# Kernel tuning notes

Hardware: AMD Instinct MI355X
Metric: run time of the kernel (lower is better)

The kernel has to match this reference:

```python
import jax, jax.numpy as jnp
import numpy as np

N, F_IN, F_OUT, N_HEAD = 4096, 256, 64, 4
EDGE_P = 0.01  # sparsity of the random adjacency


def setup_inputs() -> dict:
    key = jax.random.key(0)
    k_h, k_adj, k_w, k_as, k_ad = jax.random.split(key, 5)
    h = jax.random.normal(k_h, (N, F_IN), dtype=jnp.float32)
    # random boolean adjacency with self-loops so every softmax row is valid
    adj = jax.random.uniform(k_adj, (N, N)) < EDGE_P
    adj = adj | jnp.eye(N, dtype=bool)
    # xavier_uniform-style params
    lim_w = float(np.sqrt(6.0 / (F_IN + F_OUT)))
    lim_a = float(np.sqrt(6.0 / (F_OUT + 1)))
    w = jax.random.uniform(k_w, (N_HEAD, F_IN, F_OUT), minval=-lim_w, maxval=lim_w, dtype=jnp.float32)
    a_src = jax.random.uniform(k_as, (N_HEAD, F_OUT, 1), minval=-lim_a, maxval=lim_a, dtype=jnp.float32)
    a_dst = jax.random.uniform(k_ad, (N_HEAD, F_OUT, 1), minval=-lim_a, maxval=lim_a, dtype=jnp.float32)
    bias = jnp.zeros((F_OUT,), dtype=jnp.float32)
    return {"h": h, "adj": adj, "w": w, "a_src": a_src, "a_dst": a_dst, "bias": bias}


def reference(h, adj, w, a_src, a_dst, bias):
    # h_prime[k] = h @ w[k]  -> [H, n, f_out]
    h_prime = jnp.einsum('nf,hfo->hno', h, w)
    # attention logits: attn[k,i,j] = src[k,i] + dst[k,j]
    src = jnp.einsum('hno,ho->hn', h_prime, a_src[..., 0])  # [H, n]
    dst = jnp.einsum('hno,ho->hn', h_prime, a_dst[..., 0])  # [H, n]
    scores = src[:, :, None] + dst[:, None, :]              # [H, n, n]
    scores = jnp.where(scores >= 0, scores, 0.2 * scores)   # leaky_relu(0.2)
    neg = jnp.asarray(jnp.finfo(scores.dtype).min, scores.dtype)
    scores = jnp.where(adj[None, :, :], scores, neg)
    attn = jax.nn.softmax(scores, axis=-1)                  # [H, n, n]
    out = jnp.einsum('hij,hjo->iho', attn, h_prime)         # [n, H, f_out]
    return out + bias
```

## Files before the change

kernel.cpp:

```cpp
#include <hip/hip_runtime.h>

#define NN 4096
#define FIN 256
#define FOUT 64
#define NH 4
#define CAP 128
#define WROW 258

typedef __attribute__((ext_vector_type(8))) short bf16x8;
typedef __attribute__((ext_vector_type(4))) float f32x4;

__device__ __forceinline__ unsigned short f2bf(float f) {
    unsigned u = __float_as_uint(f);
    u = (u + 0x7fff + ((u >> 16) & 1)) >> 16;
    return (unsigned short)u;
}
__device__ __forceinline__ float bf2f(unsigned short s) {
    return __uint_as_float((unsigned)s << 16);
}
__device__ __forceinline__ int mbcnt64(unsigned long long m) {
    return __builtin_amdgcn_mbcnt_hi((unsigned)(m >> 32),
           __builtin_amdgcn_mbcnt_lo((unsigned)m, 0));
}

__global__ __launch_bounds__(256) void gat_hprime(
    const float* __restrict__ h, const float* __restrict__ w,
    const float* __restrict__ a_src, const float* __restrict__ a_dst,
    unsigned short* __restrict__ hb, float* __restrict__ sd)
{
    const int b = blockIdx.x, t = threadIdx.x;
    const int head = b & 3, n0 = (b >> 2) * 32;
    const int wv = t >> 6, lane = t & 63;
    const int lrow = lane & 15, lk8 = lane >> 4;

    __shared__ __align__(16) unsigned short ws[64 * WROW];
    __shared__ float sdbuf[2][2][16][2];

#pragma unroll
    for (int i = 0; i < 16; ++i) {
        const int k  = (t >> 4) + i * 16;
        const int o4 = (t & 15) * 4;
        const float4 v = *(const float4*)(w + ((size_t)head * FIN + k) * FOUT + o4);
        ws[(o4 + 0) * WROW + k] = f2bf(v.x);
        ws[(o4 + 1) * WROW + k] = f2bf(v.y);
        ws[(o4 + 2) * WROW + k] = f2bf(v.z);
        ws[(o4 + 3) * WROW + k] = f2bf(v.w);
    }

    const float* hrow = h + (size_t)(n0 + (wv >> 1) * 16 + lrow) * FIN + lk8 * 8;
    bf16x8 a[8];
#pragma unroll
    for (int ks = 0; ks < 8; ++ks) {
        const float4 v0 = *(const float4*)(hrow + ks * 32);
        const float4 v1 = *(const float4*)(hrow + ks * 32 + 4);
        union { bf16x8 v; unsigned short s[8]; } u;
        u.s[0] = f2bf(v0.x); u.s[1] = f2bf(v0.y);
        u.s[2] = f2bf(v0.z); u.s[3] = f2bf(v0.w);
        u.s[4] = f2bf(v1.x); u.s[5] = f2bf(v1.y);
        u.s[6] = f2bf(v1.z); u.s[7] = f2bf(v1.w);
        a[ks] = u.v;
    }
    __syncthreads();

    const int obase = (wv & 1) * 32;
    f32x4 acc[2] = {{0.f,0.f,0.f,0.f},{0.f,0.f,0.f,0.f}};
#pragma unroll
    for (int ks = 0; ks < 8; ++ks) {
#pragma unroll
        for (int nt = 0; nt < 2; ++nt) {
            const bf16x8 bf = *(const bf16x8*)
                &ws[(obase + nt * 16 + lrow) * WROW + ks * 32 + lk8 * 8];
            acc[nt] = __builtin_amdgcn_mfma_f32_16x16x32_bf16(a[ks], bf, acc[nt], 0, 0, 0);
        }
    }

    const int mbase = n0 + (wv >> 1) * 16 + lk8 * 4;
#pragma unroll
    for (int nt = 0; nt < 2; ++nt)
#pragma unroll
        for (int r = 0; r < 4; ++r)
            hb[((size_t)head * NN + mbase + r) * FOUT + obase + nt * 16 + lrow] =
                f2bf(acc[nt][r]);

    float as_nt[2], ad_nt[2];
#pragma unroll
    for (int nt = 0; nt < 2; ++nt) {
        as_nt[nt] = a_src[head * FOUT + obase + nt * 16 + lrow];
        ad_nt[nt] = a_dst[head * FOUT + obase + nt * 16 + lrow];
    }
    float psr[4] = {0.f,0.f,0.f,0.f}, pdr[4] = {0.f,0.f,0.f,0.f};
#pragma unroll
    for (int nt = 0; nt < 2; ++nt)
#pragma unroll
        for (int r = 0; r < 4; ++r) {
            psr[r] = fmaf(acc[nt][r], as_nt[nt], psr[r]);
            pdr[r] = fmaf(acc[nt][r], ad_nt[nt], pdr[r]);
        }
#pragma unroll
    for (int r = 0; r < 4; ++r)
#pragma unroll
        for (int off = 1; off <= 8; off <<= 1) {
            psr[r] += __shfl_xor(psr[r], off, 64);
            pdr[r] += __shfl_xor(pdr[r], off, 64);
        }
    if (lrow == 0)
#pragma unroll
        for (int r = 0; r < 4; ++r) {
            sdbuf[wv >> 1][wv & 1][lk8 * 4 + r][0] = psr[r];
            sdbuf[wv >> 1][wv & 1][lk8 * 4 + r][1] = pdr[r];
        }
    __syncthreads();
    if ((wv & 1) == 0 && lrow == 0) {
        const int p = wv >> 1;
#pragma unroll
        for (int r = 0; r < 4; ++r) {
            const int n = lk8 * 4 + r;
            const int node = n0 + p * 16 + n;
            sd[(size_t)node * 8 + head]     = sdbuf[p][0][n][0] + sdbuf[p][1][n][0];
            sd[(size_t)node * 8 + 4 + head] = sdbuf[p][0][n][1] + sdbuf[p][1][n][1];
        }
    }
}

__global__ __launch_bounds__(256) void gat_attn(
    const int* __restrict__ adj, const unsigned short* __restrict__ hb,
    const float* __restrict__ sd, const float* __restrict__ bias,
    float* __restrict__ out)
{
    const int i = blockIdx.x, t = threadIdx.x, wv = t >> 6, lane = t & 63;

    __shared__ int   idx_l[CAP];
    __shared__ float sc[NH][CAP];
    __shared__ int   ccnt[16];
    __shared__ float inv_sum[NH];

    const int4* arow = (const int4*)(adj + (size_t)i * NN);
    int4 a[4];
#pragma unroll
    for (int it = 0; it < 4; ++it) a[it] = arow[wv * 256 + it * 64 + lane];

    int myoff[4];
#pragma unroll
    for (int it = 0; it < 4; ++it) {
        const unsigned long long b0 = __ballot(a[it].x != 0);
        const unsigned long long b1 = __ballot(a[it].y != 0);
        const unsigned long long b2 = __ballot(a[it].z != 0);
        const unsigned long long b3 = __ballot(a[it].w != 0);
        myoff[it] = mbcnt64(b0) + mbcnt64(b1) + mbcnt64(b2) + mbcnt64(b3);
        if (lane == 0)
            ccnt[wv * 4 + it] = __popcll(b0) + __popcll(b1) +
                                __popcll(b2) + __popcll(b3);
    }
    __syncthreads();

    int cb[4];
    int s = 0;
#pragma unroll
    for (int k = 0; k < 16; ++k) {
        if ((k >> 2) == wv) cb[k & 3] = s;
        s += ccnt[k];
    }
    const int count = min(s, CAP);
    const int cpad  = (count + 7) & ~7;

#pragma unroll
    for (int it = 0; it < 4; ++it) {
        int p = cb[it] + myoff[it];
        const int col0 = (wv * 256 + it * 64 + lane) * 4;
        if (a[it].x) { if (p < CAP) idx_l[p] = col0;     ++p; }
        if (a[it].y) { if (p < CAP) idx_l[p] = col0 + 1; ++p; }
        if (a[it].z) { if (p < CAP) idx_l[p] = col0 + 2; ++p; }
        if (a[it].w) { if (p < CAP) idx_l[p] = col0 + 3; ++p; }
    }
    __syncthreads();

    if (t < count) {
        const int j = idx_l[t];
        const float4 sv = *(const float4*)(sd + (size_t)i * 8);
        const float4 dv = *(const float4*)(sd + (size_t)j * 8 + 4);
        const float s0 = sv.x + dv.x, s1 = sv.y + dv.y;
        const float s2 = sv.z + dv.z, s3 = sv.w + dv.w;
        sc[0][t] = (s0 >= 0.f) ? s0 : 0.2f * s0;
        sc[1][t] = (s1 >= 0.f) ? s1 : 0.2f * s1;
        sc[2][t] = (s2 >= 0.f) ? s2 : 0.2f * s2;
        sc[3][t] = (s3 >= 0.f) ? s3 : 0.2f * s3;
    } else if (t < cpad) {
        idx_l[t] = 0;
#pragma unroll
        for (int hh = 0; hh < NH; ++hh) sc[hh][t] = 0.f;
    }
    __syncthreads();

    {
        float m = -3.4e38f;
        for (int p = lane; p < count; p += 64) m = fmaxf(m, sc[wv][p]);
#pragma unroll
        for (int off = 32; off >= 1; off >>= 1) m = fmaxf(m, __shfl_xor(m, off, 64));
        float e = 0.f;
        for (int p = lane; p < count; p += 64) {
            const float v = __expf(sc[wv][p] - m);
            sc[wv][p] = v;
            e += v;
        }
#pragma unroll
        for (int off = 32; off >= 1; off >>= 1) e += __shfl_xor(e, off, 64);
        if (lane == 0) inv_sum[wv] = 1.f / e;
    }
    __syncthreads();

    float accv = 0.f;
    const unsigned short* hp = hb + (size_t)(wv * NN) * FOUT + lane;
    for (int p0 = 0; p0 < cpad; p0 += 8) {
        int jj[8]; unsigned short vv[8]; float ww[8];
#pragma unroll
        for (int k = 0; k < 8; ++k) jj[k] = idx_l[p0 + k];
#pragma unroll
        for (int k = 0; k < 8; ++k) vv[k] = hp[(size_t)jj[k] * FOUT];
#pragma unroll
        for (int k = 0; k < 8; ++k) ww[k] = sc[wv][p0 + k];
#pragma unroll
        for (int k = 0; k < 8; ++k) accv = fmaf(ww[k], bf2f(vv[k]), accv);
    }
    out[(size_t)i * (NH * FOUT) + wv * FOUT + lane] = accv * inv_sum[wv] + bias[lane];
}

extern "C" void kernel_launch(void* const* d_in, const int* in_sizes, int n_in,
                              void* d_out, int out_size, void* d_ws, size_t ws_size,
                              hipStream_t stream) {
    const float* h     = (const float*)d_in[0];
    const int*   adj   = (const int*)d_in[1];
    const float* w     = (const float*)d_in[2];
    const float* a_src = (const float*)d_in[3];
    const float* a_dst = (const float*)d_in[4];
    const float* bias  = (const float*)d_in[5];
    float* out = (float*)d_out;

    unsigned short* hb = (unsigned short*)d_ws;
    float* sd          = (float*)(hb + (size_t)NH * NN * FOUT);

    gat_hprime<<<512, 256, 0, stream>>>(h, w, a_src, a_dst, hb, sd);
    gat_attn<<<NN, 256, 0, stream>>>(adj, hb, sd, bias, out);
}
```

Before: 36.15 us.

## Process one attention row per wavefront and drop block-wide barriers

```diff
diff --git a/kernel.cpp b/kernel.cpp
--- a/kernel.cpp
+++ b/kernel.cpp
@@ -127,101 +127,110 @@
     const float* __restrict__ sd, const float* __restrict__ bias,
     float* __restrict__ out)
 {
-    const int i = blockIdx.x, t = threadIdx.x, wv = t >> 6, lane = t & 63;
-
-    __shared__ int   idx_l[CAP];
-    __shared__ float sc[NH][CAP];
-    __shared__ int   ccnt[16];
-    __shared__ float inv_sum[NH];
+    const int t = threadIdx.x, wv = t >> 6, lane = t & 63;
+    const int i = blockIdx.x * 4 + wv;
+
+    __shared__ int   idx_l[4][CAP];
+    __shared__ float scpk[4][CAP][4];
 
     const int4* arow = (const int4*)(adj + (size_t)i * NN);
-    int4 a[4];
-#pragma unroll
-    for (int it = 0; it < 4; ++it) a[it] = arow[wv * 256 + it * 64 + lane];
-
-    int myoff[4];
-#pragma unroll
-    for (int it = 0; it < 4; ++it) {
-        const unsigned long long b0 = __ballot(a[it].x != 0);
-        const unsigned long long b1 = __ballot(a[it].y != 0);
-        const unsigned long long b2 = __ballot(a[it].z != 0);
-        const unsigned long long b3 = __ballot(a[it].w != 0);
-        myoff[it] = mbcnt64(b0) + mbcnt64(b1) + mbcnt64(b2) + mbcnt64(b3);
-        if (lane == 0)
-            ccnt[wv * 4 + it] = __popcll(b0) + __popcll(b1) +
-                                __popcll(b2) + __popcll(b3);
-    }
-    __syncthreads();
-
-    int cb[4];
-    int s = 0;
-#pragma unroll
-    for (int k = 0; k < 16; ++k) {
-        if ((k >> 2) == wv) cb[k & 3] = s;
-        s += ccnt[k];
-    }
-    const int count = min(s, CAP);
-    const int cpad  = (count + 7) & ~7;
-
-#pragma unroll
-    for (int it = 0; it < 4; ++it) {
-        int p = cb[it] + myoff[it];
-        const int col0 = (wv * 256 + it * 64 + lane) * 4;
-        if (a[it].x) { if (p < CAP) idx_l[p] = col0;     ++p; }
-        if (a[it].y) { if (p < CAP) idx_l[p] = col0 + 1; ++p; }
-        if (a[it].z) { if (p < CAP) idx_l[p] = col0 + 2; ++p; }
-        if (a[it].w) { if (p < CAP) idx_l[p] = col0 + 3; ++p; }
-    }
-    __syncthreads();
-
-    if (t < count) {
-        const int j = idx_l[t];
-        const float4 sv = *(const float4*)(sd + (size_t)i * 8);
-        const float4 dv = *(const float4*)(sd + (size_t)j * 8 + 4);
-        const float s0 = sv.x + dv.x, s1 = sv.y + dv.y;
-        const float s2 = sv.z + dv.z, s3 = sv.w + dv.w;
-        sc[0][t] = (s0 >= 0.f) ? s0 : 0.2f * s0;
-        sc[1][t] = (s1 >= 0.f) ? s1 : 0.2f * s1;
-        sc[2][t] = (s2 >= 0.f) ? s2 : 0.2f * s2;
-        sc[3][t] = (s3 >= 0.f) ? s3 : 0.2f * s3;
-    } else if (t < cpad) {
-        idx_l[t] = 0;
-#pragma unroll
-        for (int hh = 0; hh < NH; ++hh) sc[hh][t] = 0.f;
-    }
-    __syncthreads();
-
+    int run = 0;
+#pragma unroll
+    for (int half = 0; half < 2; ++half) {
+        int4 v[8];
+#pragma unroll
+        for (int it = 0; it < 8; ++it) v[it] = arow[(half * 8 + it) * 64 + lane];
+#pragma unroll
+        for (int it = 0; it < 8; ++it) {
+            const unsigned long long b0 = __ballot(v[it].x != 0);
+            const unsigned long long b1 = __ballot(v[it].y != 0);
+            const unsigned long long b2 = __ballot(v[it].z != 0);
+            const unsigned long long b3 = __ballot(v[it].w != 0);
+            int p = run + mbcnt64(b0) + mbcnt64(b1) + mbcnt64(b2) + mbcnt64(b3);
+            const int col0 = ((half * 8 + it) * 64 + lane) * 4;
+            if (v[it].x) { if (p < CAP) idx_l[wv][p] = col0;     ++p; }
+            if (v[it].y) { if (p < CAP) idx_l[wv][p] = col0 + 1; ++p; }
+            if (v[it].z) { if (p < CAP) idx_l[wv][p] = col0 + 2; ++p; }
+            if (v[it].w) { if (p < CAP) idx_l[wv][p] = col0 + 3; ++p; }
+            run += __popcll(b0) + __popcll(b1) + __popcll(b2) + __popcll(b3);
+        }
+    }
+    const int count = min(run, CAP);
+    asm volatile("" ::: "memory");
+
+    const float4 sv = *(const float4*)(sd + (size_t)i * 8);
+    const bool actA = lane < count, actB = lane + 64 < count;
+    const int jA = actA ? idx_l[wv][lane] : 0;
+    const int jB = actB ? idx_l[wv][lane + 64] : 0;
+    const float4 dvA = *(const float4*)(sd + (size_t)jA * 8 + 4);
+    const float4 dvB = *(const float4*)(sd + (size_t)jB * 8 + 4);
+
+    float sA[4], sB[4];
     {
-        float m = -3.4e38f;
-        for (int p = lane; p < count; p += 64) m = fmaxf(m, sc[wv][p]);
-#pragma unroll
-        for (int off = 32; off >= 1; off >>= 1) m = fmaxf(m, __shfl_xor(m, off, 64));
-        float e = 0.f;
-        for (int p = lane; p < count; p += 64) {
-            const float v = __expf(sc[wv][p] - m);
-            sc[wv][p] = v;
-            e += v;
-        }
-#pragma unroll
-        for (int off = 32; off >= 1; off >>= 1) e += __shfl_xor(e, off, 64);
-        if (lane == 0) inv_sum[wv] = 1.f / e;
-    }
-    __syncthreads();
-
-    float accv = 0.f;
-    const unsigned short* hp = hb + (size_t)(wv * NN) * FOUT + lane;
-    for (int p0 = 0; p0 < cpad; p0 += 8) {
-        int jj[8]; unsigned short vv[8]; float ww[8];
-#pragma unroll
-        for (int k = 0; k < 8; ++k) jj[k] = idx_l[p0 + k];
-#pragma unroll
-        for (int k = 0; k < 8; ++k) vv[k] = hp[(size_t)jj[k] * FOUT];
-#pragma unroll
-        for (int k = 0; k < 8; ++k) ww[k] = sc[wv][p0 + k];
-#pragma unroll
-        for (int k = 0; k < 8; ++k) accv = fmaf(ww[k], bf2f(vv[k]), accv);
-    }
-    out[(size_t)i * (NH * FOUT) + wv * FOUT + lane] = accv * inv_sum[wv] + bias[lane];
+        const float a0 = sv.x + dvA.x, a1 = sv.y + dvA.y,
+                    a2 = sv.z + dvA.z, a3 = sv.w + dvA.w;
+        const float b0 = sv.x + dvB.x, b1 = sv.y + dvB.y,
+                    b2 = sv.z + dvB.z, b3 = sv.w + dvB.w;
+        sA[0] = actA ? ((a0 >= 0.f) ? a0 : 0.2f * a0) : -3.4e38f;
+        sA[1] = actA ? ((a1 >= 0.f) ? a1 : 0.2f * a1) : -3.4e38f;
+        sA[2] = actA ? ((a2 >= 0.f) ? a2 : 0.2f * a2) : -3.4e38f;
+        sA[3] = actA ? ((a3 >= 0.f) ? a3 : 0.2f * a3) : -3.4e38f;
+        sB[0] = actB ? ((b0 >= 0.f) ? b0 : 0.2f * b0) : -3.4e38f;
+        sB[1] = actB ? ((b1 >= 0.f) ? b1 : 0.2f * b1) : -3.4e38f;
+        sB[2] = actB ? ((b2 >= 0.f) ? b2 : 0.2f * b2) : -3.4e38f;
+        sB[3] = actB ? ((b3 >= 0.f) ? b3 : 0.2f * b3) : -3.4e38f;
+    }
+
+    float m[4], eA[4], eB[4], inv[4];
+#pragma unroll
+    for (int hh = 0; hh < 4; ++hh) {
+        float mm = fmaxf(sA[hh], sB[hh]);
+#pragma unroll
+        for (int off = 32; off >= 1; off >>= 1)
+            mm = fmaxf(mm, __shfl_xor(mm, off, 64));
+        m[hh] = mm;
+        eA[hh] = actA ? __expf(sA[hh] - mm) : 0.f;
+        eB[hh] = actB ? __expf(sB[hh] - mm) : 0.f;
+        float e = eA[hh] + eB[hh];
+#pragma unroll
+        for (int off = 32; off >= 1; off >>= 1)
+            e += __shfl_xor(e, off, 64);
+        inv[hh] = 1.f / e;
+    }
+
+    if (actA) *(float4*)&scpk[wv][lane][0]      = make_float4(eA[0], eA[1], eA[2], eA[3]);
+    if (actB) *(float4*)&scpk[wv][lane + 64][0] = make_float4(eB[0], eB[1], eB[2], eB[3]);
+    asm volatile("" ::: "memory");
+
+    float acc[4] = {0.f, 0.f, 0.f, 0.f};
+    const unsigned short* hpb = hb + lane;
+    for (int p0 = 0; p0 < count; p0 += 4) {
+        int jj[4]; float wts[4][4]; unsigned short hv[4][4];
+#pragma unroll
+        for (int k = 0; k < 4; ++k) {
+            const int pp = p0 + k;
+            const bool act = pp < count;
+            jj[k] = act ? idx_l[wv][pp] : 0;
+            const float4 wt = act ? *(const float4*)&scpk[wv][pp][0]
+                                  : make_float4(0.f, 0.f, 0.f, 0.f);
+            wts[k][0] = wt.x; wts[k][1] = wt.y; wts[k][2] = wt.z; wts[k][3] = wt.w;
+        }
+#pragma unroll
+        for (int k = 0; k < 4; ++k)
+#pragma unroll
+            for (int hh = 0; hh < 4; ++hh)
+                hv[k][hh] = hpb[((size_t)(hh * NN) + jj[k]) * FOUT];
+#pragma unroll
+        for (int k = 0; k < 4; ++k)
+#pragma unroll
+            for (int hh = 0; hh < 4; ++hh)
+                acc[hh] = fmaf(wts[k][hh], bf2f(hv[k][hh]), acc[hh]);
+    }
+
+    const float bv = bias[lane];
+#pragma unroll
+    for (int hh = 0; hh < 4; ++hh)
+        out[(size_t)i * (NH * FOUT) + hh * FOUT + lane] = acc[hh] * inv[hh] + bv;
 }
 
 extern "C" void kernel_launch(void* const* d_in, const int* in_sizes, int n_in,
@@ -239,5 +248,5 @@
     float* sd          = (float*)(hb + (size_t)NH * NN * FOUT);
 
     gat_hprime<<<512, 256, 0, stream>>>(h, w, a_src, a_dst, hb, sd);
-    gat_attn<<<NN, 256, 0, stream>>>(adj, hb, sd, bias, out);
-}
+    gat_attn<<<NN / 4, 256, 0, stream>>>(adj, hb, sd, bias, out);
+}
```

Measured after the change: 39.19 us. +8.4%, slower.

## Split neighbor aggregation across waves with vectorized 4-wide bf16 gathers and LDS reduction

Applied to the files above, without the earlier changes.

```diff
diff --git a/kernel.cpp b/kernel.cpp
--- a/kernel.cpp
+++ b/kernel.cpp
@@ -133,6 +133,7 @@
     __shared__ float sc[NH][CAP];
     __shared__ int   ccnt[16];
     __shared__ float inv_sum[NH];
+    __shared__ float accbuf[4][64][4];
 
     const int4* arow = (const int4*)(adj + (size_t)i * NN);
     int4 a[4];
@@ -161,7 +162,6 @@
         s += ccnt[k];
     }
     const int count = min(s, CAP);
-    const int cpad  = (count + 7) & ~7;
 
 #pragma unroll
     for (int it = 0; it < 4; ++it) {
@@ -184,10 +184,6 @@
         sc[1][t] = (s1 >= 0.f) ? s1 : 0.2f * s1;
         sc[2][t] = (s2 >= 0.f) ? s2 : 0.2f * s2;
         sc[3][t] = (s3 >= 0.f) ? s3 : 0.2f * s3;
-    } else if (t < cpad) {
-        idx_l[t] = 0;
-#pragma unroll
-        for (int hh = 0; hh < NH; ++hh) sc[hh][t] = 0.f;
     }
     __syncthreads();
 
@@ -208,20 +204,50 @@
     }
     __syncthreads();
 
-    float accv = 0.f;
-    const unsigned short* hp = hb + (size_t)(wv * NN) * FOUT + lane;
-    for (int p0 = 0; p0 < cpad; p0 += 8) {
-        int jj[8]; unsigned short vv[8]; float ww[8];
-#pragma unroll
-        for (int k = 0; k < 8; ++k) jj[k] = idx_l[p0 + k];
-#pragma unroll
-        for (int k = 0; k < 8; ++k) vv[k] = hp[(size_t)jj[k] * FOUT];
-#pragma unroll
-        for (int k = 0; k < 8; ++k) ww[k] = sc[wv][p0 + k];
-#pragma unroll
-        for (int k = 0; k < 8; ++k) accv = fmaf(ww[k], bf2f(vv[k]), accv);
-    }
-    out[(size_t)i * (NH * FOUT) + wv * FOUT + lane] = accv * inv_sum[wv] + bias[lane];
+    const int hh = lane >> 4, og = lane & 15;
+    const unsigned short* hpb = hb + (size_t)hh * NN * FOUT + og * 4;
+    float4 accv = make_float4(0.f, 0.f, 0.f, 0.f);
+    for (int p0 = wv; p0 < count; p0 += 16) {
+        int jj[4]; float ee[4]; ushort4 hv[4];
+#pragma unroll
+        for (int k = 0; k < 4; ++k) {
+            const int pp = p0 + k * 4;
+            const bool act = pp < count;
+            jj[k] = act ? idx_l[pp] : 0;
+            ee[k] = act ? sc[hh][pp] : 0.f;
+        }
+#pragma unroll
+        for (int k = 0; k < 4; ++k)
+            hv[k] = *(const ushort4*)(hpb + (size_t)jj[k] * FOUT);
+#pragma unroll
+        for (int k = 0; k < 4; ++k) {
+            accv.x = fmaf(ee[k], bf2f(hv[k].x), accv.x);
+            accv.y = fmaf(ee[k], bf2f(hv[k].y), accv.y);
+            accv.z = fmaf(ee[k], bf2f(hv[k].z), accv.z);
+            accv.w = fmaf(ee[k], bf2f(hv[k].w), accv.w);
+        }
+    }
+    *(float4*)&accbuf[wv][lane][0] = accv;
+    __syncthreads();
+
+    if (wv == 0) {
+        float4 r0 = *(const float4*)&accbuf[0][lane][0];
+        const float4 r1 = *(const float4*)&accbuf[1][lane][0];
+        const float4 r2 = *(const float4*)&accbuf[2][lane][0];
+        const float4 r3 = *(const float4*)&accbuf[3][lane][0];
+        r0.x += r1.x + r2.x + r3.x;
+        r0.y += r1.y + r2.y + r3.y;
+        r0.z += r1.z + r2.z + r3.z;
+        r0.w += r1.w + r2.w + r3.w;
+        const float is = inv_sum[hh];
+        const float4 bv = *(const float4*)(bias + og * 4);
+        float4 o;
+        o.x = r0.x * is + bv.x;
+        o.y = r0.y * is + bv.y;
+        o.z = r0.z * is + bv.z;
+        o.w = r0.w * is + bv.w;
+        *(float4*)(out + (size_t)i * (NH * FOUT) + hh * FOUT + og * 4) = o;
+    }
 }
 
 extern "C" void kernel_launch(void* const* d_in, const int* in_sizes, int n_in,
```

After: 34.65 us. 1.04x faster.

## Process four rows per attention block with double-buffered adjacency prefetch

Applied to the files above, without the earlier changes.

```diff
diff --git a/kernel.cpp b/kernel.cpp
--- a/kernel.cpp
+++ b/kernel.cpp
@@ -21,6 +21,10 @@
 __device__ __forceinline__ int mbcnt64(unsigned long long m) {
     return __builtin_amdgcn_mbcnt_hi((unsigned)(m >> 32),
            __builtin_amdgcn_mbcnt_lo((unsigned)m, 0));
+}
+__device__ __forceinline__ void wg_barrier() {
+    asm volatile("s_waitcnt lgkmcnt(0)" ::: "memory");
+    __builtin_amdgcn_s_barrier();
 }
 
 __global__ __launch_bounds__(256) void gat_hprime(
@@ -122,106 +126,148 @@
     }
 }
 
+#define LOADROW(BUF, RR) do {                                              \
+    const int4* arow_ = (const int4*)(adj + (size_t)(RR) * NN);            \
+    _Pragma("unroll")                                                      \
+    for (int it_ = 0; it_ < 4; ++it_)                                      \
+        BUF[it_] = arow_[wv * 256 + it_ * 64 + lane];                      \
+} while (0)
+
+#define TAIL(BUF, RR) do {                                                 \
+    int myoff_[4];                                                         \
+    _Pragma("unroll")                                                      \
+    for (int it_ = 0; it_ < 4; ++it_) {                                    \
+        const unsigned long long b0_ = __ballot(BUF[it_].x != 0);          \
+        const unsigned long long b1_ = __ballot(BUF[it_].y != 0);          \
+        const unsigned long long b2_ = __ballot(BUF[it_].z != 0);          \
+        const unsigned long long b3_ = __ballot(BUF[it_].w != 0);          \
+        myoff_[it_] = mbcnt64(b0_) + mbcnt64(b1_) + mbcnt64(b2_) + mbcnt64(b3_); \
+        if (lane == 0)                                                     \
+            ccnt[wv * 4 + it_] = __popcll(b0_) + __popcll(b1_) +           \
+                                 __popcll(b2_) + __popcll(b3_);            \
+    }                                                                      \
+    wg_barrier();                                                          \
+    int cb_[4];                                                            \
+    int s_ = 0;                                                            \
+    _Pragma("unroll")                                                      \
+    for (int k_ = 0; k_ < 16; ++k_) {                                      \
+        if ((k_ >> 2) == wv) cb_[k_ & 3] = s_;                             \
+        s_ += ccnt[k_];                                                    \
+    }                                                                      \
+    const int count_ = min(s_, CAP);                                       \
+    _Pragma("unroll")                                                      \
+    for (int it_ = 0; it_ < 4; ++it_) {                                    \
+        int p_ = cb_[it_] + myoff_[it_];                                   \
+        const int col0_ = (wv * 256 + it_ * 64 + lane) * 4;                \
+        if (BUF[it_].x) { if (p_ < CAP) idx_l[p_] = col0_;     ++p_; }     \
+        if (BUF[it_].y) { if (p_ < CAP) idx_l[p_] = col0_ + 1; ++p_; }     \
+        if (BUF[it_].z) { if (p_ < CAP) idx_l[p_] = col0_ + 2; ++p_; }     \
+        if (BUF[it_].w) { if (p_ < CAP) idx_l[p_] = col0_ + 3; ++p_; }     \
+    }                                                                      \
+    wg_barrier();                                                          \
+    if (t < count_) {                                                      \
+        const int j_ = idx_l[t];                                           \
+        const float4 sv_ = *(const float4*)(sd + (size_t)(RR) * 8);        \
+        const float4 dv_ = *(const float4*)(sd + (size_t)j_ * 8 + 4);      \
+        const float s0_ = sv_.x + dv_.x, s1_ = sv_.y + dv_.y;              \
+        const float s2_ = sv_.z + dv_.z, s3_ = sv_.w + dv_.w;              \
+        sc[0][t] = (s0_ >= 0.f) ? s0_ : 0.2f * s0_;                        \
+        sc[1][t] = (s1_ >= 0.f) ? s1_ : 0.2f * s1_;                        \
+        sc[2][t] = (s2_ >= 0.f) ? s2_ : 0.2f * s2_;                        \
+        sc[3][t] = (s3_ >= 0.f) ? s3_ : 0.2f * s3_;                        \
+    }                                                                      \
+    wg_barrier();                                                          \
+    {                                                                      \
+        float m_ = -3.4e38f;                                               \
+        for (int p_ = lane; p_ < count_; p_ += 64)                         \
+            m_ = fmaxf(m_, sc[wv][p_]);                                    \
+        _Pragma("unroll")                                                  \
+        for (int off_ = 32; off_ >= 1; off_ >>= 1)                         \
+            m_ = fmaxf(m_, __shfl_xor(m_, off_, 64));                      \
+        float e_ = 0.f;                                                    \
+        for (int p_ = lane; p_ < count_; p_ += 64) {                       \
+            const float v_ = __expf(sc[wv][p_] - m_);                      \
+            sc[wv][p_] = v_;                                               \
+            e_ += v_;                                                      \
+        }                                                                  \
+        _Pragma("unroll")                                                  \
+        for (int off_ = 32; off_ >= 1; off_ >>= 1)                         \
+            e_ += __shfl_xor(e_, off_, 64);                                \
+        if (lane == 0) inv_sum[wv] = 1.f / e_;                             \
+    }                                                                      \
+    wg_barrier();                                                          \
+    {                                                                      \
+        const int hh_ = lane >> 4, og_ = lane & 15;                        \
+        const unsigned short* hpb_ = hb + (size_t)hh_ * NN * FOUT + og_ * 4; \
+        float4 accv_ = make_float4(0.f, 0.f, 0.f, 0.f);                    \
+        for (int p0_ = wv; p0_ < count_; p0_ += 16) {                      \
+            int jj_[4]; float ee_[4]; ushort4 hv_[4];                      \
+            _Pragma("unroll")                                              \
+            for (int k_ = 0; k_ < 4; ++k_) {                               \
+                const int pp_ = p0_ + k_ * 4;                              \
+                const bool act_ = pp_ < count_;                            \
+                jj_[k_] = act_ ? idx_l[pp_] : 0;                           \
+                ee_[k_] = act_ ? sc[hh_][pp_] : 0.f;                       \
+            }                                                              \
+            _Pragma("unroll")                                              \
+            for (int k_ = 0; k_ < 4; ++k_)                                 \
+                hv_[k_] = *(const ushort4*)(hpb_ + (size_t)jj_[k_] * FOUT); \
+            _Pragma("unroll")                                              \
+            for (int k_ = 0; k_ < 4; ++k_) {                               \
+                accv_.x = fmaf(ee_[k_], bf2f(hv_[k_].x), accv_.x);         \
+                accv_.y = fmaf(ee_[k_], bf2f(hv_[k_].y), accv_.y);         \
+                accv_.z = fmaf(ee_[k_], bf2f(hv_[k_].z), accv_.z);         \
+                accv_.w = fmaf(ee_[k_], bf2f(hv_[k_].w), accv_.w);         \
+            }                                                              \
+        }                                                                  \
+        *(float4*)&accbuf[wv][lane][0] = accv_;                            \
+    }                                                                      \
+    wg_barrier();                                                          \
+    if (wv == 0) {                                                         \
+        const int hh_ = lane >> 4, og_ = lane & 15;                        \
+        float4 r0_ = *(const float4*)&accbuf[0][lane][0];                  \
+        const float4 r1_ = *(const float4*)&accbuf[1][lane][0];            \
+        const float4 r2_ = *(const float4*)&accbuf[2][lane][0];            \
+        const float4 r3_ = *(const float4*)&accbuf[3][lane][0];            \
+        r0_.x += r1_.x + r2_.x + r3_.x;                                    \
+        r0_.y += r1_.y + r2_.y + r3_.y;                                    \
+        r0_.z += r1_.z + r2_.z + r3_.z;                                    \
+        r0_.w += r1_.w + r2_.w + r3_.w;                                    \
+        const float is_ = inv_sum[hh_];                                    \
+        const float4 bv_ = *(const float4*)(bias + og_ * 4);               \
+        float4 o_;                                                         \
+        o_.x = r0_.x * is_ + bv_.x;                                        \
+        o_.y = r0_.y * is_ + bv_.y;                                        \
+        o_.z = r0_.z * is_ + bv_.z;                                        \
+        o_.w = r0_.w * is_ + bv_.w;                                        \
+        *(float4*)(out + (size_t)(RR) * (NH * FOUT) + hh_ * FOUT + og_ * 4) = o_; \
+    }                                                                      \
+    wg_barrier();                                                          \
+} while (0)
+
 __global__ __launch_bounds__(256) void gat_attn(
     const int* __restrict__ adj, const unsigned short* __restrict__ hb,
     const float* __restrict__ sd, const float* __restrict__ bias,
     float* __restrict__ out)
 {
-    const int i = blockIdx.x, t = threadIdx.x, wv = t >> 6, lane = t & 63;
+    const int t = threadIdx.x, wv = t >> 6, lane = t & 63;
+    const int r0 = blockIdx.x * 4;
 
     __shared__ int   idx_l[CAP];
     __shared__ float sc[NH][CAP];
     __shared__ int   ccnt[16];
     __shared__ float inv_sum[NH];
-
-    const int4* arow = (const int4*)(adj + (size_t)i * NN);
-    int4 a[4];
-#pragma unroll
-    for (int it = 0; it < 4; ++it) a[it] = arow[wv * 256 + it * 64 + lane];
-
-    int myoff[4];
-#pragma unroll
-    for (int it = 0; it < 4; ++it) {
-        const unsigned long long b0 = __ballot(a[it].x != 0);
-        const unsigned long long b1 = __ballot(a[it].y != 0);
-        const unsigned long long b2 = __ballot(a[it].z != 0);
-        const unsigned long long b3 = __ballot(a[it].w != 0);
-        myoff[it] = mbcnt64(b0) + mbcnt64(b1) + mbcnt64(b2) + mbcnt64(b3);
-        if (lane == 0)
-            ccnt[wv * 4 + it] = __popcll(b0) + __popcll(b1) +
-                                __popcll(b2) + __popcll(b3);
-    }
-    __syncthreads();
-
-    int cb[4];
-    int s = 0;
-#pragma unroll
-    for (int k = 0; k < 16; ++k) {
-        if ((k >> 2) == wv) cb[k & 3] = s;
-        s += ccnt[k];
-    }
-    const int count = min(s, CAP);
-    const int cpad  = (count + 7) & ~7;
-
-#pragma unroll
-    for (int it = 0; it < 4; ++it) {
-        int p = cb[it] + myoff[it];
-        const int col0 = (wv * 256 + it * 64 + lane) * 4;
-        if (a[it].x) { if (p < CAP) idx_l[p] = col0;     ++p; }
-        if (a[it].y) { if (p < CAP) idx_l[p] = col0 + 1; ++p; }
-        if (a[it].z) { if (p < CAP) idx_l[p] = col0 + 2; ++p; }
-        if (a[it].w) { if (p < CAP) idx_l[p] = col0 + 3; ++p; }
-    }
-    __syncthreads();
-
-    if (t < count) {
-        const int j = idx_l[t];
-        const float4 sv = *(const float4*)(sd + (size_t)i * 8);
-        const float4 dv = *(const float4*)(sd + (size_t)j * 8 + 4);
-        const float s0 = sv.x + dv.x, s1 = sv.y + dv.y;
-        const float s2 = sv.z + dv.z, s3 = sv.w + dv.w;
-        sc[0][t] = (s0 >= 0.f) ? s0 : 0.2f * s0;
-        sc[1][t] = (s1 >= 0.f) ? s1 : 0.2f * s1;
-        sc[2][t] = (s2 >= 0.f) ? s2 : 0.2f * s2;
-        sc[3][t] = (s3 >= 0.f) ? s3 : 0.2f * s3;
-    } else if (t < cpad) {
-        idx_l[t] = 0;
-#pragma unroll
-        for (int hh = 0; hh < NH; ++hh) sc[hh][t] = 0.f;
-    }
-    __syncthreads();
-
-    {
-        float m = -3.4e38f;
-        for (int p = lane; p < count; p += 64) m = fmaxf(m, sc[wv][p]);
-#pragma unroll
-        for (int off = 32; off >= 1; off >>= 1) m = fmaxf(m, __shfl_xor(m, off, 64));
-        float e = 0.f;
-        for (int p = lane; p < count; p += 64) {
-            const float v = __expf(sc[wv][p] - m);
-            sc[wv][p] = v;
-            e += v;
-        }
-#pragma unroll
-        for (int off = 32; off >= 1; off >>= 1) e += __shfl_xor(e, off, 64);
-        if (lane == 0) inv_sum[wv] = 1.f / e;
-    }
-    __syncthreads();
-
-    float accv = 0.f;
-    const unsigned short* hp = hb + (size_t)(wv * NN) * FOUT + lane;
-    for (int p0 = 0; p0 < cpad; p0 += 8) {
-        int jj[8]; unsigned short vv[8]; float ww[8];
-#pragma unroll
-        for (int k = 0; k < 8; ++k) jj[k] = idx_l[p0 + k];
-#pragma unroll
-        for (int k = 0; k < 8; ++k) vv[k] = hp[(size_t)jj[k] * FOUT];
-#pragma unroll
-        for (int k = 0; k < 8; ++k) ww[k] = sc[wv][p0 + k];
-#pragma unroll
-        for (int k = 0; k < 8; ++k) accv = fmaf(ww[k], bf2f(vv[k]), accv);
-    }
-    out[(size_t)i * (NH * FOUT) + wv * FOUT + lane] = accv * inv_sum[wv] + bias[lane];
+    __shared__ float accbuf[4][64][4];
+
+    int4 A[4], B[4];
+    LOADROW(A, r0);
+    LOADROW(B, r0 + 1);
+    TAIL(A, r0);
+    LOADROW(A, r0 + 2);
+    TAIL(B, r0 + 1);
+    LOADROW(B, r0 + 3);
+    TAIL(A, r0 + 2);
+    TAIL(B, r0 + 3);
 }
 
 extern "C" void kernel_launch(void* const* d_in, const int* in_sizes, int n_in,
@@ -239,5 +285,5 @@
     float* sd          = (float*)(hb + (size_t)NH * NN * FOUT);
 
     gat_hprime<<<512, 256, 0, stream>>>(h, w, a_src, a_dst, hb, sd);
-    gat_attn<<<NN, 256, 0, stream>>>(adj, hb, sd, bias, out);
-}
+    gat_attn<<<NN / 4, 256, 0, stream>>>(adj, hb, sd, bias, out);
+}
```

New measurement: 40.02 us. +10.7%, slower.
